# Kernel tuning notes

Hardware: AMD Instinct MI355X
Metric: run time of the kernel (lower is better)

The kernel has to match this reference:

```python
import jax, jax.numpy as jnp
import numpy as np

E = 768
NH_REG = 6   # num_heads - cultural_heads
NH_CUL = 2   # cultural_heads


def _branch(x, wq, bq, wk, bk, wv, bv, wo, bo, cb, nh, mask_add):
    # x: [B,T,E]; weights stored as [in,out]; cb: [1,nh,1,hd]
    B, T, Edim = x.shape
    hd = Edim // nh
    scale = hd ** -0.5
    q = (x @ wq + bq).reshape(B, T, nh, hd).transpose(0, 2, 1, 3)
    k = (x @ wk + bk).reshape(B, T, nh, hd).transpose(0, 2, 1, 3)
    v = (x @ wv + bv).reshape(B, T, nh, hd).transpose(0, 2, 1, 3)
    q = q + cb  # learned cultural bias added to Q
    scores = jnp.einsum('bhtd,bhsd->bhts', q, k) * scale
    scores = scores + mask_add
    w = jax.nn.softmax(scores, axis=-1)  # dropout omitted (eval mode)
    out = jnp.einsum('bhts,bhsd->bhtd', w, v)
    out = out.transpose(0, 2, 1, 3).reshape(B, T, Edim)
    return out @ wo + bo


def setup_inputs() -> dict:
    key = jax.random.key(0)
    ks = jax.random.split(key, 24)
    B, S = 2, 2048
    d = {
        'hidden_states': jax.random.normal(ks[0], (B, S, E), jnp.float32),
        'cultural_mask': jax.random.normal(ks[1], (B, S, S), jnp.float32),
        'attention_mask': jax.random.normal(ks[2], (B, 1, 1, S), jnp.float32),
    }
    s = E ** -0.5
    names = ['rq_w', 'rk_w', 'rv_w', 'ro_w', 'cq_w', 'ck_w', 'cv_w', 'co_w']
    for i, n in enumerate(names):
        d[n] = jax.random.normal(ks[3 + i], (E, E), jnp.float32) * s
    for i, n in enumerate(['rq_b', 'rk_b', 'rv_b', 'ro_b', 'cq_b', 'ck_b', 'cv_b', 'co_b']):
        d[n] = jax.random.normal(ks[11 + i], (E,), jnp.float32) * 0.02
    d['r_cb'] = jnp.zeros((1, NH_REG, 1, E // NH_REG), jnp.float32)
    d['c_cb'] = jnp.zeros((1, NH_CUL, 1, E // NH_CUL), jnp.float32)
    # NOTE: concat of two branches gives 2E features -> out layer maps 2E -> E
    d['out_w'] = jax.random.normal(ks[19], (2 * E, E), jnp.float32) * (2 * E) ** -0.5
    d['out_b'] = jax.random.normal(ks[20], (E,), jnp.float32) * 0.02
    return d


def reference(hidden_states, cultural_mask, attention_mask,
              rq_w, rk_w, rv_w, ro_w, cq_w, ck_w, cv_w, co_w,
              rq_b, rk_b, rv_b, ro_b, cq_b, ck_b, cv_b, co_b,
              r_cb, c_cb, out_w, out_b):
    # regular branch: attention_mask only
    reg = _branch(hidden_states, rq_w, rq_b, rk_w, rk_b, rv_w, rv_b,
                  ro_w, ro_b, r_cb, NH_REG, attention_mask)
    # cultural branch: cultural_mask (broadcast over heads) + attention_mask
    cmask = cultural_mask[:, None, :, :] + attention_mask
    cul = _branch(hidden_states, cq_w, cq_b, ck_w, ck_b, cv_w, cv_b,
                  co_w, co_b, c_cb, NH_CUL, cmask)
    combined = jnp.concatenate([reg, cul], axis=-1)  # [B,T,2E]
    return combined @ out_w + out_b
```

## Files before the change

kernel.cpp:

```cpp
#include <hip/hip_runtime.h>
#include <hip/hip_bf16.h>

using u16 = unsigned short;
using u32 = unsigned int;
typedef short short8 __attribute__((ext_vector_type(8)));
typedef float f32x4 __attribute__((ext_vector_type(4)));

#define B_  2
#define S_  2048
#define E_  768
#define BS_ 4096

#define L2E_ 1.44269504088896f
#define FML2_ 17.3123404906676f

__device__ __forceinline__ u16 f2bf(float f) {
  __hip_bfloat16 h = __float2bfloat16(f);
  return *reinterpret_cast<u16*>(&h);
}

__device__ __forceinline__ u32 pk2(float a, float b) {
  return (u32)f2bf(a) | ((u32)f2bf(b) << 16);
}

__device__ __forceinline__ void gld16(const void* g, void* l) {
  __builtin_amdgcn_global_load_lds(
      (const __attribute__((address_space(1))) u32*)g,
      (__attribute__((address_space(3))) u32*)l, 16, 0, 0);
}


__global__ __launch_bounds__(256) void conv_x_k(const float* __restrict__ x,
                                                u16* __restrict__ xb, int n4) {
  int i = blockIdx.x * 256 + threadIdx.x;
  if (i >= n4) return;
  float4 v = reinterpret_cast<const float4*>(x)[i];
  reinterpret_cast<uint2*>(xb)[i] = make_uint2(pk2(v.x, v.y), pk2(v.z, v.w));
}

__global__ __launch_bounds__(256) void bias_k(
    const float* rqb, const float* rkb, const float* rvb,
    const float* cqb, const float* ckb, const float* cvb,
    const float* rob, const float* cob,
    const float* rcb, const float* ccb,
    float* bqkv, float* bproj) {
  int t = blockIdx.x * 256 + threadIdx.x;
  if (t < 4608) {
    int seg = t / 768, i = t - seg * 768;
    float v = 0.f;
    if      (seg == 0) v = rqb[i] + rcb[i];
    else if (seg == 1) v = rkb[i];
    else if (seg == 2) v = rvb[i];
    else if (seg == 3) v = cqb[i] + ccb[i];
    else if (seg == 4) v = ckb[i];
    else               v = cvb[i];
    bqkv[t] = v;
  } else {
    int u = t - 4608;
    if (u < 1536) bproj[u] = (u < 768) ? rob[u] : cob[u - 768];
  }
}

struct TP {
  const float* src[9];
  u16* dst[9];
  int rows[9];
};

__global__ __launch_bounds__(256) void transpose_k(TP p) {
  int mi = blockIdx.z;
  int rows = p.rows[mi];
  int r0 = blockIdx.y * 32;
  if (r0 >= rows) return;
  int c0 = blockIdx.x * 32;
  const float* src = p.src[mi];
  u16* dst = p.dst[mi];
  __shared__ float t[32][33];
  int tx = threadIdx.x & 31, ty = threadIdx.x >> 5;
#pragma unroll
  for (int d = 0; d < 4; ++d) {
    int r = ty + d * 8;
    t[r][tx] = src[(size_t)(r0 + r) * 768 + c0 + tx];
  }
  __syncthreads();
#pragma unroll
  for (int d = 0; d < 4; ++d) {
    int c = ty + d * 8;
    dst[(size_t)(c0 + c) * rows + r0 + tx] = f2bf(t[tx][c]);
  }
}


template<int MODE>
__global__ __launch_bounds__(256) void gemm_t_k(
    const u16* __restrict__ A, int lda,
    const u16* __restrict__ BT, int ldb,
    const float* __restrict__ bias, int K,
    const u16* __restrict__ A2, int msplit, int bofs,
    void* __restrict__ Cout, int ldc,
    u16* __restrict__ Qr, u16* __restrict__ Kr, u16* __restrict__ Vtr,
    u16* __restrict__ Qc, u16* __restrict__ Kc, u16* __restrict__ Vtc) {
  __shared__ u16 lA[128 * 32];
  __shared__ u16 lB[128 * 32];
  const int tid = threadIdx.x, w = tid >> 6, lane = tid & 63;
  const int quad = lane >> 4, l15 = lane & 15;
  const int m0 = blockIdx.y * 128, n0 = blockIdx.x * 128;
  if (msplit && m0 >= msplit) { A = A2 - (size_t)msplit * lda; BT += bofs; }

  const f32x4 z4 = {0.f, 0.f, 0.f, 0.f};
  f32x4 acc[4][4];
#pragma unroll
  for (int i = 0; i < 4; ++i)
#pragma unroll
    for (int j = 0; j < 4; ++j) acc[i][j] = z4;

  const int sr = w * 32 + (lane >> 2);
  const int scp = lane & 3;

  for (int kt = 0; kt < K; kt += 32) {
    int r1 = sr, r2 = sr + 16;
    int c1 = (scp - (r1 >> 2)) & 3;
    int c2 = (scp - (r2 >> 2)) & 3;
    gld16(A + (size_t)(m0 + r1) * lda + kt + c1 * 8, &lA[r1 * 32 + scp * 8]);
    gld16(A + (size_t)(m0 + r2) * lda + kt + c2 * 8, &lA[r2 * 32 + scp * 8]);
    gld16(BT + (size_t)(n0 + r1) * ldb + kt + c1 * 8, &lB[r1 * 32 + scp * 8]);
    gld16(BT + (size_t)(n0 + r2) * ldb + kt + c2 * 8, &lB[r2 * 32 + scp * 8]);
    __syncthreads();
    short8 af[4], bg[4];
#pragma unroll
    for (int i = 0; i < 4; ++i) {
      int r = (w >> 1) * 64 + i * 16 + l15;
      af[i] = *reinterpret_cast<const short8*>(&lA[r * 32 + ((quad + (r >> 2)) & 3) * 8]);
    }
#pragma unroll
    for (int j = 0; j < 4; ++j) {
      int r = (w & 1) * 64 + j * 16 + l15;
      bg[j] = *reinterpret_cast<const short8*>(&lB[r * 32 + ((quad + (r >> 2)) & 3) * 8]);
    }
#pragma unroll
    for (int i = 0; i < 4; ++i)
#pragma unroll
      for (int j = 0; j < 4; ++j)
        acc[i][j] = __builtin_amdgcn_mfma_f32_16x16x32_bf16(af[i], bg[j], acc[i][j], 0, 0, 0);
    __syncthreads();
  }

  const int seg = (MODE == 2) ? (m0 / 768) : 0;
#pragma unroll
  for (int i = 0; i < 4; ++i) {
    int f = m0 + (w >> 1) * 64 + i * 16 + quad * 4;
    float4 b4 = *reinterpret_cast<const float4*>(bias + f);
#pragma unroll
    for (int j = 0; j < 4; ++j) {
      int t = n0 + (w & 1) * 64 + j * 16 + l15;
      float v0 = acc[i][j][0] + b4.x;
      float v1 = acc[i][j][1] + b4.y;
      float v2 = acc[i][j][2] + b4.z;
      float v3 = acc[i][j][3] + b4.w;
      if (MODE == 0) {
        *reinterpret_cast<uint2*>((u16*)Cout + (size_t)t * ldc + f) =
            make_uint2(pk2(v0, v1), pk2(v2, v3));
      } else if (MODE == 1) {
        *reinterpret_cast<float4*>((float*)Cout + (size_t)t * ldc + f) =
            make_float4(v0, v1, v2, v3);
      } else {
        int b = t >> 11, s = t & 2047;
        int fs = f - seg * 768;
        if (seg == 0) {
          int h = fs >> 7, d = fs & 127;
          *reinterpret_cast<uint2*>(Qr + ((size_t)(b * 6 + h) * 2048 + s) * 128 + d) =
              make_uint2(pk2(v0, v1), pk2(v2, v3));
        } else if (seg == 1) {
          int h = fs >> 7, d = fs & 127;
          *reinterpret_cast<uint2*>(Kr + ((size_t)(b * 6 + h) * 2048 + s) * 128 + d) =
              make_uint2(pk2(v0, v1), pk2(v2, v3));
        } else if (seg == 2) {
          int h = fs >> 7, d = fs & 127;
          u16* vp = Vtr + ((size_t)(b * 6 + h) * 128 + d) * 2048 + s;
          vp[0] = f2bf(v0); vp[2048] = f2bf(v1); vp[4096] = f2bf(v2); vp[6144] = f2bf(v3);
        } else if (seg == 3) {
          int h = fs / 384, d = fs - h * 384;
          *reinterpret_cast<uint2*>(Qc + ((size_t)(b * 2 + h) * 2048 + s) * 384 + d) =
              make_uint2(pk2(v0, v1), pk2(v2, v3));
        } else if (seg == 4) {
          int h = fs / 384, d = fs - h * 384;
          *reinterpret_cast<uint2*>(Kc + ((size_t)(b * 2 + h) * 2048 + s) * 384 + d) =
              make_uint2(pk2(v0, v1), pk2(v2, v3));
        } else {
          int h = fs / 384, d = fs - h * 384;
          u16* vp = Vtc + ((size_t)(b * 2 + h) * 384 + d) * 2048 + s;
          vp[0] = f2bf(v0); vp[2048] = f2bf(v1); vp[4096] = f2bf(v2); vp[6144] = f2bf(v3);
        }
      }
    }
  }
}

__global__ __launch_bounds__(256) void attn_freg_k(
    const u16* __restrict__ Qr, const u16* __restrict__ Kr,
    const u16* __restrict__ Vtr, const float* __restrict__ am,
    u16* __restrict__ AO, float scl) {
  __shared__ u16 lQ[64 * 128];
  __shared__ u16 lK[128 * 32];
  __shared__ u16 lV[128 * 32];
  __shared__ u16 lP[64 * 128];
  __shared__ float lL[2][64];

  const int tid = threadIdx.x, w = tid >> 6, lane = tid & 63;
  const int quad = lane >> 4, l15 = lane & 15;
  const int L = blockIdx.x;
  const int gg = (L & 7) * 48 + (L >> 3);
  const int bh = gg >> 5;
  const int q0 = (gg & 31) * 64;
  const int b = bh / 6, h = bh - b * 6;

  const u16* Qb = Qr + ((size_t)bh * S_ + q0) * 128;
  const u16* Kb0 = Kr + (size_t)bh * S_ * 128;
  const u16* Vb0 = Vtr + (size_t)bh * 128 * S_;
  const float* amb = am + b * S_;

#pragma unroll
  for (int it = 0; it < 4; ++it) {
    int idx = it * 256 + tid;
    int row = idx >> 4, gs = idx & 15;
    gld16(Qb + (size_t)row * 128 + (size_t)(gs ^ (row & 15)) * 8, &lQ[idx * 8]);
  }

  const f32x4 z4 = {0.f, 0.f, 0.f, 0.f};
  f32x4 accO[4][2];
#pragma unroll
  for (int i = 0; i < 4; ++i)
#pragma unroll
    for (int j = 0; j < 2; ++j) accO[i][j] = z4;
  float lsum[2] = {0.f, 0.f};

  const int sr = w * 32 + (lane >> 2);
  const int scp = lane & 3;
  const int r1 = sr, r2 = sr + 16;
  const int c1 = (scp - (r1 >> 2)) & 3;
  const int c2 = (scp - (r2 >> 2)) & 3;
  const int khalf = w >> 1, qhalf = w & 1;

  for (int t = 0; t < 16; ++t) {
    const u16* Kb = Kb0 + (size_t)(t * 128) * 128;
    f32x4 accS[4][2];
#pragma unroll
    for (int i = 0; i < 4; ++i)
#pragma unroll
      for (int j = 0; j < 2; ++j) accS[i][j] = z4;

#pragma unroll
    for (int c = 0; c < 4; ++c) {
      gld16(Kb + (size_t)r1 * 128 + c * 32 + c1 * 8, &lK[r1 * 32 + scp * 8]);
      gld16(Kb + (size_t)r2 * 128 + c * 32 + c2 * 8, &lK[r2 * 32 + scp * 8]);
      __syncthreads();
      short8 af[4], bg[2];
#pragma unroll
      for (int i = 0; i < 4; ++i) {
        int r = khalf * 64 + i * 16 + l15;
        af[i] = *reinterpret_cast<const short8*>(&lK[r * 32 + ((quad + (r >> 2)) & 3) * 8]);
      }
#pragma unroll
      for (int j = 0; j < 2; ++j) {
        int q = qhalf * 32 + j * 16 + l15;
        int s = (4 * c + quad) ^ (q & 15);
        bg[j] = *reinterpret_cast<const short8*>(&lQ[q * 128 + s * 8]);
      }
#pragma unroll
      for (int i = 0; i < 4; ++i)
#pragma unroll
        for (int j = 0; j < 2; ++j)
          accS[i][j] = __builtin_amdgcn_mfma_f32_16x16x32_bf16(af[i], bg[j], accS[i][j], 0, 0, 0);
      __syncthreads();
    }

#pragma unroll
    for (int i = 0; i < 4; ++i) {
      int kb = khalf * 64 + i * 16 + quad * 4;
      float4 a4 = *reinterpret_cast<const float4*>(amb + t * 128 + kb);
      float p0c = fmaf(a4.x, L2E_, -FML2_);
      float p1c = fmaf(a4.y, L2E_, -FML2_);
      float p2c = fmaf(a4.z, L2E_, -FML2_);
      float p3c = fmaf(a4.w, L2E_, -FML2_);
      int sg = (kb >> 3) ^ 0;
      int so = kb & 7;
#pragma unroll
      for (int j = 0; j < 2; ++j) {
        int q = qhalf * 32 + j * 16 + l15;
        float p0 = exp2f(fmaf(accS[i][j][0], scl, p0c));
        float p1 = exp2f(fmaf(accS[i][j][1], scl, p1c));
        float p2 = exp2f(fmaf(accS[i][j][2], scl, p2c));
        float p3 = exp2f(fmaf(accS[i][j][3], scl, p3c));
        lsum[j] += (p0 + p1) + (p2 + p3);
        int s = ((kb >> 3) ^ (q & 15));
        *reinterpret_cast<uint2*>(&lP[q * 128 + s * 8 + so]) =
            make_uint2(pk2(p0, p1), pk2(p2, p3));
      }
      (void)sg;
    }
    __syncthreads();

    const u16* Vb = Vb0 + t * 128;
#pragma unroll
    for (int c = 0; c < 4; ++c) {
      gld16(Vb + (size_t)r1 * S_ + c * 32 + c1 * 8, &lV[r1 * 32 + scp * 8]);
      gld16(Vb + (size_t)r2 * S_ + c * 32 + c2 * 8, &lV[r2 * 32 + scp * 8]);
      __syncthreads();
      short8 af[4], bg[2];
#pragma unroll
      for (int i = 0; i < 4; ++i) {
        int r = khalf * 64 + i * 16 + l15;
        af[i] = *reinterpret_cast<const short8*>(&lV[r * 32 + ((quad + (r >> 2)) & 3) * 8]);
      }
#pragma unroll
      for (int j = 0; j < 2; ++j) {
        int q = qhalf * 32 + j * 16 + l15;
        int s = (4 * c + quad) ^ (q & 15);
        bg[j] = *reinterpret_cast<const short8*>(&lP[q * 128 + s * 8]);
      }
#pragma unroll
      for (int i = 0; i < 4; ++i)
#pragma unroll
        for (int j = 0; j < 2; ++j)
          accO[i][j] = __builtin_amdgcn_mfma_f32_16x16x32_bf16(af[i], bg[j], accO[i][j], 0, 0, 0);
      __syncthreads();
    }
  }

#pragma unroll
  for (int j = 0; j < 2; ++j) {
    float s = lsum[j];
    s += __shfl_xor(s, 16);
    s += __shfl_xor(s, 32);
    if (lane < 16) lL[khalf][qhalf * 32 + j * 16 + lane] = s;
  }
  __syncthreads();

  float invl[2];
#pragma unroll
  for (int j = 0; j < 2; ++j) {
    int q = qhalf * 32 + j * 16 + l15;
    invl[j] = 1.f / (lL[0][q] + lL[1][q]);
  }
#pragma unroll
  for (int i = 0; i < 4; ++i) {
    int d = khalf * 64 + i * 16 + quad * 4;
#pragma unroll
    for (int j = 0; j < 2; ++j) {
      int tok = q0 + qhalf * 32 + j * 16 + l15;
      float v0 = accO[i][j][0] * invl[j];
      float v1 = accO[i][j][1] * invl[j];
      float v2 = accO[i][j][2] * invl[j];
      float v3 = accO[i][j][3] * invl[j];
      *reinterpret_cast<uint2*>(AO + ((size_t)(b * S_ + tok)) * 1536 + h * 128 + d) =
          make_uint2(pk2(v0, v1), pk2(v2, v3));
    }
  }
}

__global__ __launch_bounds__(256) void attn_g1_k(
    const u16* __restrict__ Qr, const u16* __restrict__ Kr,
    const u16* __restrict__ Qc, const u16* __restrict__ Kc,
    u16* __restrict__ Pr, u16* __restrict__ Pc, float* __restrict__ Lp,
    const float* __restrict__ am, const float* __restrict__ cmask,
    float sReg, float sCul, int zoff) {
  __shared__ u16 lA[128 * 32];
  __shared__ u16 lB[128 * 32];
  const int tid = threadIdx.x, w = tid >> 6, lane = tid & 63;
  const int quad = lane >> 4, l15 = lane & 15;
  const int m0 = blockIdx.y * 128, n0 = blockIdx.x * 128;
  const int gz = zoff + blockIdx.z;
  const u16 *A, *BT;
  u16* P;
  const float* cm = nullptr;
  float scl;
  int K, b;
  if (gz < 12) {
    A = Kr + (size_t)gz * S_ * 128;
    BT = Qr + (size_t)gz * S_ * 128;
    K = 128;
    P = Pr + (size_t)blockIdx.z * (size_t)S_ * S_;
    scl = sReg;
    b = gz / 6;
  } else {
    int hc = gz - 12;
    A = Kc + (size_t)hc * S_ * 384;
    BT = Qc + (size_t)hc * S_ * 384;
    K = 384;
    P = Pc + (size_t)hc * (size_t)S_ * S_;
    b = hc >> 1;
    cm = cmask + (size_t)b * S_ * S_;
    scl = sCul;
  }

  const f32x4 z4 = {0.f, 0.f, 0.f, 0.f};
  f32x4 acc[4][4];
#pragma unroll
  for (int i = 0; i < 4; ++i)
#pragma unroll
    for (int j = 0; j < 4; ++j) acc[i][j] = z4;

  const int sr = w * 32 + (lane >> 2);
  const int scp = lane & 3;

  for (int kt = 0; kt < K; kt += 32) {
    int r1 = sr, r2 = sr + 16;
    int c1 = (scp - (r1 >> 2)) & 3;
    int c2 = (scp - (r2 >> 2)) & 3;
    gld16(A + (size_t)(m0 + r1) * K + kt + c1 * 8, &lA[r1 * 32 + scp * 8]);
    gld16(A + (size_t)(m0 + r2) * K + kt + c2 * 8, &lA[r2 * 32 + scp * 8]);
    gld16(BT + (size_t)(n0 + r1) * K + kt + c1 * 8, &lB[r1 * 32 + scp * 8]);
    gld16(BT + (size_t)(n0 + r2) * K + kt + c2 * 8, &lB[r2 * 32 + scp * 8]);
    __syncthreads();
    short8 af[4], bg[4];
#pragma unroll
    for (int i = 0; i < 4; ++i) {
      int r = (w >> 1) * 64 + i * 16 + l15;
      af[i] = *reinterpret_cast<const short8*>(&lA[r * 32 + ((quad + (r >> 2)) & 3) * 8]);
    }
#pragma unroll
    for (int j = 0; j < 4; ++j) {
      int r = (w & 1) * 64 + j * 16 + l15;
      bg[j] = *reinterpret_cast<const short8*>(&lB[r * 32 + ((quad + (r >> 2)) & 3) * 8]);
    }
#pragma unroll
    for (int i = 0; i < 4; ++i)
#pragma unroll
      for (int j = 0; j < 4; ++j)
        acc[i][j] = __builtin_amdgcn_mfma_f32_16x16x32_bf16(af[i], bg[j], acc[i][j], 0, 0, 0);
    __syncthreads();
  }

  const float* amb = am + b * S_;
  float lsum[4] = {0.f, 0.f, 0.f, 0.f};
#pragma unroll
  for (int i = 0; i < 4; ++i) {
    int kb = m0 + (w >> 1) * 64 + i * 16 + quad * 4;
    float4 a4 = *reinterpret_cast<const float4*>(amb + kb);
    float pre0 = fmaf(a4.x, L2E_, -FML2_);
    float pre1 = fmaf(a4.y, L2E_, -FML2_);
    float pre2 = fmaf(a4.z, L2E_, -FML2_);
    float pre3 = fmaf(a4.w, L2E_, -FML2_);
#pragma unroll
    for (int j = 0; j < 4; ++j) {
      int q = n0 + (w & 1) * 64 + j * 16 + l15;
      float c0 = pre0, c1 = pre1, c2 = pre2, c3 = pre3;
      if (cm) {
        float4 cmv = *reinterpret_cast<const float4*>(cm + (size_t)q * S_ + kb);
        c0 = fmaf(cmv.x, L2E_, c0);
        c1 = fmaf(cmv.y, L2E_, c1);
        c2 = fmaf(cmv.z, L2E_, c2);
        c3 = fmaf(cmv.w, L2E_, c3);
      }
      float p0 = exp2f(fmaf(acc[i][j][0], scl, c0));
      float p1 = exp2f(fmaf(acc[i][j][1], scl, c1));
      float p2 = exp2f(fmaf(acc[i][j][2], scl, c2));
      float p3 = exp2f(fmaf(acc[i][j][3], scl, c3));
      lsum[j] += (p0 + p1) + (p2 + p3);
      *reinterpret_cast<uint2*>(P + (size_t)q * S_ + kb) =
          make_uint2(pk2(p0, p1), pk2(p2, p3));
    }
  }
#pragma unroll
  for (int j = 0; j < 4; ++j) {
    float s = lsum[j];
    s += __shfl_xor(s, 16);
    s += __shfl_xor(s, 32);
    if (lane < 16)
      Lp[(size_t)gz * (32 * S_) + ((size_t)((m0 >> 7) * 2 + (w >> 1))) * S_ +
         n0 + (w & 1) * 64 + j * 16 + lane] = s;
  }
}

__global__ __launch_bounds__(256) void attn_g2_k(
    const u16* __restrict__ Pr, const u16* __restrict__ Pc,
    const u16* __restrict__ Vtr, const u16* __restrict__ Vtc,
    const float* __restrict__ Lp, u16* __restrict__ AO, int zoff) {
  const int gz = zoff + blockIdx.z;
  const int m0 = blockIdx.y * 128, n0 = blockIdx.x * 128;
  const u16 *A, *BT;
  int b, colbase;
  if (gz < 12) {
    if (blockIdx.y) return;
    A = Vtr + (size_t)gz * 128 * S_;
    BT = Pr + (size_t)blockIdx.z * (size_t)S_ * S_;
    b = gz / 6;
    colbase = (gz % 6) * 128;
  } else {
    int hc = gz - 12;
    A = Vtc + (size_t)hc * 384 * S_;
    BT = Pc + (size_t)hc * (size_t)S_ * S_;
    b = hc >> 1;
    colbase = 768 + (hc & 1) * 384;
  }
  __shared__ u16 lA[128 * 32];
  __shared__ u16 lB[128 * 32];
  __shared__ float lL[128];
  const int tid = threadIdx.x, w = tid >> 6, lane = tid & 63;
  const int quad = lane >> 4, l15 = lane & 15;

  if (tid < 128) {
    const float* lp = Lp + (size_t)gz * (32 * S_) + (n0 + tid);
    float s = 0.f;
#pragma unroll
    for (int g = 0; g < 32; ++g) s += lp[(size_t)g * S_];
    lL[tid] = 1.f / s;
  }

  const f32x4 z4 = {0.f, 0.f, 0.f, 0.f};
  f32x4 acc[4][4];
#pragma unroll
  for (int i = 0; i < 4; ++i)
#pragma unroll
    for (int j = 0; j < 4; ++j) acc[i][j] = z4;

  const int sr = w * 32 + (lane >> 2);
  const int scp = lane & 3;

  for (int kt = 0; kt < S_; kt += 32) {
    int r1 = sr, r2 = sr + 16;
    int c1 = (scp - (r1 >> 2)) & 3;
    int c2 = (scp - (r2 >> 2)) & 3;
    gld16(A + (size_t)(m0 + r1) * S_ + kt + c1 * 8, &lA[r1 * 32 + scp * 8]);
    gld16(A + (size_t)(m0 + r2) * S_ + kt + c2 * 8, &lA[r2 * 32 + scp * 8]);
    gld16(BT + (size_t)(n0 + r1) * S_ + kt + c1 * 8, &lB[r1 * 32 + scp * 8]);
    gld16(BT + (size_t)(n0 + r2) * S_ + kt + c2 * 8, &lB[r2 * 32 + scp * 8]);
    __syncthreads();
    short8 af[4], bg[4];
#pragma unroll
    for (int i = 0; i < 4; ++i) {
      int r = (w >> 1) * 64 + i * 16 + l15;
      af[i] = *reinterpret_cast<const short8*>(&lA[r * 32 + ((quad + (r >> 2)) & 3) * 8]);
    }
#pragma unroll
    for (int j = 0; j < 4; ++j) {
      int r = (w & 1) * 64 + j * 16 + l15;
      bg[j] = *reinterpret_cast<const short8*>(&lB[r * 32 + ((quad + (r >> 2)) & 3) * 8]);
    }
#pragma unroll
    for (int i = 0; i < 4; ++i)
#pragma unroll
      for (int j = 0; j < 4; ++j)
        acc[i][j] = __builtin_amdgcn_mfma_f32_16x16x32_bf16(af[i], bg[j], acc[i][j], 0, 0, 0);
    __syncthreads();
  }

  float invl[4];
#pragma unroll
  for (int j = 0; j < 4; ++j) invl[j] = lL[(w & 1) * 64 + j * 16 + l15];
#pragma unroll
  for (int i = 0; i < 4; ++i) {
    int feat = colbase + m0 + (w >> 1) * 64 + i * 16 + quad * 4;
#pragma unroll
    for (int j = 0; j < 4; ++j) {
      int q = n0 + (w & 1) * 64 + j * 16 + l15;
      float v0 = acc[i][j][0] * invl[j];
      float v1 = acc[i][j][1] * invl[j];
      float v2 = acc[i][j][2] * invl[j];
      float v3 = acc[i][j][3] * invl[j];
      *reinterpret_cast<uint2*>(AO + ((size_t)(b * S_ + q)) * 1536 + feat) =
          make_uint2(pk2(v0, v1), pk2(v2, v3));
    }
  }
}


extern "C" void kernel_launch(void* const* d_in, const int* in_sizes, int n_in,
                              void* d_out, int out_size, void* d_ws, size_t ws_size,
                              hipStream_t stream) {
  const float* x     = (const float*)d_in[0];
  const float* cmask = (const float*)d_in[1];
  const float* amask = (const float*)d_in[2];
  const float* W[8]  = { (const float*)d_in[3], (const float*)d_in[4], (const float*)d_in[5],
                         (const float*)d_in[6], (const float*)d_in[7], (const float*)d_in[8],
                         (const float*)d_in[9], (const float*)d_in[10] };
  const float* rq_b = (const float*)d_in[11];
  const float* rk_b = (const float*)d_in[12];
  const float* rv_b = (const float*)d_in[13];
  const float* ro_b = (const float*)d_in[14];
  const float* cq_b = (const float*)d_in[15];
  const float* ck_b = (const float*)d_in[16];
  const float* cv_b = (const float*)d_in[17];
  const float* co_b = (const float*)d_in[18];
  const float* r_cb = (const float*)d_in[19];
  const float* c_cb = (const float*)d_in[20];
  const float* out_w = (const float*)d_in[21];
  const float* out_b = (const float*)d_in[22];

  char* p = (char*)d_ws;
  auto carve = [&](size_t bytes) -> void* {
    void* r = (void*)p;
    p += (bytes + 255) & ~(size_t)255;
    return r;
  };
  u16* Xb    = (u16*)carve((size_t)BS_ * E_ * 2);
  u16* WqkvT = (u16*)carve((size_t)4608 * 768 * 2);
  u16* roT   = (u16*)carve((size_t)768 * 768 * 2);
  u16* coT   = (u16*)carve((size_t)768 * 768 * 2);
  u16* outwT = (u16*)carve((size_t)768 * 1536 * 2);
  float* bqkv  = (float*)carve(4608 * 4);
  float* bproj = (float*)carve(1536 * 4);
  u16* Qr  = (u16*)carve((size_t)B_ * 6 * S_ * 128 * 2);
  u16* Kr  = (u16*)carve((size_t)B_ * 6 * S_ * 128 * 2);
  u16* Vtr = (u16*)carve((size_t)B_ * 6 * S_ * 128 * 2);
  u16* Qc  = (u16*)carve((size_t)B_ * 2 * S_ * 384 * 2);
  u16* Kc  = (u16*)carve((size_t)B_ * 2 * S_ * 384 * 2);
  u16* Vtc = (u16*)carve((size_t)B_ * 2 * S_ * 384 * 2);
  u16* AO  = (u16*)carve((size_t)BS_ * 1536 * 2);

  float* Lp = (float*)Xb;
  u16* Pcul = (u16*)carve((size_t)4 * S_ * S_ * 2);
  u16* PR = Pcul;

  const float sReg = 0.08838834764831845f * L2E_;
  const float sCul = 0.05103103630798288f * L2E_;

  conv_x_k<<<dim3(BS_ * E_ / 4 / 256), 256, 0, stream>>>(x, Xb, BS_ * E_ / 4);
  bias_k<<<dim3(24), 256, 0, stream>>>(rq_b, rk_b, rv_b, cq_b, ck_b, cv_b,
                                       ro_b, co_b, r_cb, c_cb, bqkv, bproj);

  TP tp;
  const int wsel[6] = {0, 1, 2, 4, 5, 6};
  for (int i = 0; i < 6; ++i) {
    tp.src[i] = W[wsel[i]];
    tp.dst[i] = WqkvT + (size_t)i * 768 * 768;
    tp.rows[i] = 768;
  }
  tp.src[6] = W[3]; tp.dst[6] = roT;   tp.rows[6] = 768;
  tp.src[7] = W[7]; tp.dst[7] = coT;   tp.rows[7] = 768;
  tp.src[8] = out_w; tp.dst[8] = outwT; tp.rows[8] = 1536;
  transpose_k<<<dim3(24, 48, 9), 256, 0, stream>>>(tp);

  gemm_t_k<2><<<dim3(32, 36), 256, 0, stream>>>(
      WqkvT, 768, Xb, 768, bqkv, 768,
      (const u16*)nullptr, 0, 0, (void*)nullptr, 0,
      Qr, Kr, Vtr, Qc, Kc, Vtc);

  attn_freg_k<<<dim3(384), 256, 0, stream>>>(Qr, Kr, Vtr, amask, AO, sReg);

  attn_g1_k<<<dim3(16, 16, 4), 256, 0, stream>>>(
      Qr, Kr, Qc, Kc, (u16*)nullptr, Pcul, Lp, amask, cmask, sReg, sCul, 12);
  attn_g2_k<<<dim3(16, 3, 4), 256, 0, stream>>>(
      (const u16*)nullptr, Pcul, Vtr, Vtc, Lp, AO, 12);

  gemm_t_k<0><<<dim3(32, 12), 256, 0, stream>>>(
      roT, 768, AO, 1536, bproj, 768,
      coT, 768, 768, (void*)PR, 1536,
      nullptr, nullptr, nullptr, nullptr, nullptr, nullptr);

  gemm_t_k<1><<<dim3(32, 6), 256, 0, stream>>>(
      outwT, 1536, PR, 1536, out_b, 1536,
      (const u16*)nullptr, 0, 0, d_out, 768,
      nullptr, nullptr, nullptr, nullptr, nullptr, nullptr);
}
```

Before: 426.7 us.

## Fold output projections into final weight and load regular-attention fragments from global

```diff
diff --git a/kernel.cpp b/kernel.cpp
--- a/kernel.cpp
+++ b/kernel.cpp
@@ -17,6 +17,11 @@
 __device__ __forceinline__ u16 f2bf(float f) {
   __hip_bfloat16 h = __float2bfloat16(f);
   return *reinterpret_cast<u16*>(&h);
+}
+
+__device__ __forceinline__ float bf2f(u16 b) {
+  u32 bits = (u32)b << 16;
+  return *reinterpret_cast<float*>(&bits);
 }
 
 __device__ __forceinline__ u32 pk2(float a, float b) {
@@ -38,12 +43,26 @@
   reinterpret_cast<uint2*>(xb)[i] = make_uint2(pk2(v.x, v.y), pk2(v.z, v.w));
 }
 
+__global__ __launch_bounds__(256) void conv_w_k(const float* __restrict__ ro,
+                                                const float* __restrict__ co,
+                                                u16* __restrict__ roB,
+                                                u16* __restrict__ coB) {
+  const int n4 = 768 * 768 / 4;
+  int i = blockIdx.x * 256 + threadIdx.x;
+  const float* src = (i < n4) ? ro : co;
+  u16* dst = (i < n4) ? roB : coB;
+  int k = (i < n4) ? i : i - n4;
+  if (k >= n4) return;
+  float4 v = reinterpret_cast<const float4*>(src)[k];
+  reinterpret_cast<uint2*>(dst)[k] = make_uint2(pk2(v.x, v.y), pk2(v.z, v.w));
+}
+
 __global__ __launch_bounds__(256) void bias_k(
     const float* rqb, const float* rkb, const float* rvb,
     const float* cqb, const float* ckb, const float* cvb,
     const float* rob, const float* cob,
     const float* rcb, const float* ccb,
-    float* bqkv, float* bproj) {
+    float* bqkv, float* bproj, float* zb) {
   int t = blockIdx.x * 256 + threadIdx.x;
   if (t < 4608) {
     int seg = t / 768, i = t - seg * 768;
@@ -55,10 +74,29 @@
     else if (seg == 4) v = ckb[i];
     else               v = cvb[i];
     bqkv[t] = v;
-  } else {
+  } else if (t < 6144) {
     int u = t - 4608;
-    if (u < 1536) bproj[u] = (u < 768) ? rob[u] : cob[u - 768];
-  }
+    bproj[u] = (u < 768) ? rob[u] : cob[u - 768];
+  } else if (t < 6912) {
+    zb[t - 6144] = 0.f;
+  }
+}
+
+__global__ __launch_bounds__(64) void bfin_k(
+    const float* __restrict__ bproj, const u16* __restrict__ outwT,
+    const float* __restrict__ outb, float* __restrict__ bfin) {
+  int o = blockIdx.x;
+  int lane = threadIdx.x;
+  const u16* row = outwT + (size_t)o * 1536;
+  float s = 0.f;
+  for (int i = lane; i < 1536; i += 64) s += bproj[i] * bf2f(row[i]);
+  s += __shfl_xor(s, 1);
+  s += __shfl_xor(s, 2);
+  s += __shfl_xor(s, 4);
+  s += __shfl_xor(s, 8);
+  s += __shfl_xor(s, 16);
+  s += __shfl_xor(s, 32);
+  if (lane == 0) bfin[o] = s + outb[o];
 }
 
 struct TP {
@@ -200,9 +238,6 @@
     const u16* __restrict__ Qr, const u16* __restrict__ Kr,
     const u16* __restrict__ Vtr, const float* __restrict__ am,
     u16* __restrict__ AO, float scl) {
-  __shared__ u16 lQ[64 * 128];
-  __shared__ u16 lK[128 * 32];
-  __shared__ u16 lV[128 * 32];
   __shared__ u16 lP[64 * 128];
   __shared__ float lL[2][64];
 
@@ -213,18 +248,20 @@
   const int bh = gg >> 5;
   const int q0 = (gg & 31) * 64;
   const int b = bh / 6, h = bh - b * 6;
+  const int khalf = w >> 1, qhalf = w & 1;
 
   const u16* Qb = Qr + ((size_t)bh * S_ + q0) * 128;
   const u16* Kb0 = Kr + (size_t)bh * S_ * 128;
   const u16* Vb0 = Vtr + (size_t)bh * 128 * S_;
   const float* amb = am + b * S_;
 
-#pragma unroll
-  for (int it = 0; it < 4; ++it) {
-    int idx = it * 256 + tid;
-    int row = idx >> 4, gs = idx & 15;
-    gld16(Qb + (size_t)row * 128 + (size_t)(gs ^ (row & 15)) * 8, &lQ[idx * 8]);
-  }
+  short8 qf[2][4];
+#pragma unroll
+  for (int j = 0; j < 2; ++j)
+#pragma unroll
+    for (int c = 0; c < 4; ++c)
+      qf[j][c] = *reinterpret_cast<const short8*>(
+          Qb + (size_t)(qhalf * 32 + j * 16 + l15) * 128 + c * 32 + quad * 8);
 
   const f32x4 z4 = {0.f, 0.f, 0.f, 0.f};
   f32x4 accO[4][2];
@@ -234,45 +271,28 @@
     for (int j = 0; j < 2; ++j) accO[i][j] = z4;
   float lsum[2] = {0.f, 0.f};
 
-  const int sr = w * 32 + (lane >> 2);
-  const int scp = lane & 3;
-  const int r1 = sr, r2 = sr + 16;
-  const int c1 = (scp - (r1 >> 2)) & 3;
-  const int c2 = (scp - (r2 >> 2)) & 3;
-  const int khalf = w >> 1, qhalf = w & 1;
-
   for (int t = 0; t < 16; ++t) {
-    const u16* Kb = Kb0 + (size_t)(t * 128) * 128;
     f32x4 accS[4][2];
 #pragma unroll
     for (int i = 0; i < 4; ++i)
 #pragma unroll
       for (int j = 0; j < 2; ++j) accS[i][j] = z4;
-
+    const u16* Kt = Kb0 + (size_t)t * 128 * 128;
 #pragma unroll
     for (int c = 0; c < 4; ++c) {
-      gld16(Kb + (size_t)r1 * 128 + c * 32 + c1 * 8, &lK[r1 * 32 + scp * 8]);
-      gld16(Kb + (size_t)r2 * 128 + c * 32 + c2 * 8, &lK[r2 * 32 + scp * 8]);
-      __syncthreads();
-      short8 af[4], bg[2];
-#pragma unroll
-      for (int i = 0; i < 4; ++i) {
-        int r = khalf * 64 + i * 16 + l15;
-        af[i] = *reinterpret_cast<const short8*>(&lK[r * 32 + ((quad + (r >> 2)) & 3) * 8]);
-      }
-#pragma unroll
-      for (int j = 0; j < 2; ++j) {
-        int q = qhalf * 32 + j * 16 + l15;
-        int s = (4 * c + quad) ^ (q & 15);
-        bg[j] = *reinterpret_cast<const short8*>(&lQ[q * 128 + s * 8]);
-      }
+      short8 kf[4];
 #pragma unroll
       for (int i = 0; i < 4; ++i)
+        kf[i] = *reinterpret_cast<const short8*>(
+            Kt + (size_t)(khalf * 64 + i * 16 + l15) * 128 + c * 32 + quad * 8);
+#pragma unroll
+      for (int i = 0; i < 4; ++i)
 #pragma unroll
         for (int j = 0; j < 2; ++j)
-          accS[i][j] = __builtin_amdgcn_mfma_f32_16x16x32_bf16(af[i], bg[j], accS[i][j], 0, 0, 0);
-      __syncthreads();
-    }
+          accS[i][j] = __builtin_amdgcn_mfma_f32_16x16x32_bf16(kf[i], qf[j][c], accS[i][j], 0, 0, 0);
+    }
+
+    __syncthreads();
 
 #pragma unroll
     for (int i = 0; i < 4; ++i) {
@@ -282,8 +302,6 @@
       float p1c = fmaf(a4.y, L2E_, -FML2_);
       float p2c = fmaf(a4.z, L2E_, -FML2_);
       float p3c = fmaf(a4.w, L2E_, -FML2_);
-      int sg = (kb >> 3) ^ 0;
-      int so = kb & 7;
 #pragma unroll
       for (int j = 0; j < 2; ++j) {
         int q = qhalf * 32 + j * 16 + l15;
@@ -293,25 +311,20 @@
         float p3 = exp2f(fmaf(accS[i][j][3], scl, p3c));
         lsum[j] += (p0 + p1) + (p2 + p3);
         int s = ((kb >> 3) ^ (q & 15));
-        *reinterpret_cast<uint2*>(&lP[q * 128 + s * 8 + so]) =
+        *reinterpret_cast<uint2*>(&lP[q * 128 + s * 8 + (kb & 7)]) =
             make_uint2(pk2(p0, p1), pk2(p2, p3));
       }
-      (void)sg;
-    }
-    __syncthreads();
-
-    const u16* Vb = Vb0 + t * 128;
+    }
+    __syncthreads();
+
 #pragma unroll
     for (int c = 0; c < 4; ++c) {
-      gld16(Vb + (size_t)r1 * S_ + c * 32 + c1 * 8, &lV[r1 * 32 + scp * 8]);
-      gld16(Vb + (size_t)r2 * S_ + c * 32 + c2 * 8, &lV[r2 * 32 + scp * 8]);
-      __syncthreads();
-      short8 af[4], bg[2];
-#pragma unroll
-      for (int i = 0; i < 4; ++i) {
-        int r = khalf * 64 + i * 16 + l15;
-        af[i] = *reinterpret_cast<const short8*>(&lV[r * 32 + ((quad + (r >> 2)) & 3) * 8]);
-      }
+      short8 vf[4];
+#pragma unroll
+      for (int i = 0; i < 4; ++i)
+        vf[i] = *reinterpret_cast<const short8*>(
+            Vb0 + (size_t)(khalf * 64 + i * 16 + l15) * S_ + t * 128 + c * 32 + quad * 8);
+      short8 bg[2];
 #pragma unroll
       for (int j = 0; j < 2; ++j) {
         int q = qhalf * 32 + j * 16 + l15;
@@ -322,8 +335,7 @@
       for (int i = 0; i < 4; ++i)
 #pragma unroll
         for (int j = 0; j < 2; ++j)
-          accO[i][j] = __builtin_amdgcn_mfma_f32_16x16x32_bf16(af[i], bg[j], accO[i][j], 0, 0, 0);
-      __syncthreads();
+          accO[i][j] = __builtin_amdgcn_mfma_f32_16x16x32_bf16(vf[i], bg[j], accO[i][j], 0, 0, 0);
     }
   }
 
@@ -359,39 +371,23 @@
 }
 
 __global__ __launch_bounds__(256) void attn_g1_k(
-    const u16* __restrict__ Qr, const u16* __restrict__ Kr,
     const u16* __restrict__ Qc, const u16* __restrict__ Kc,
-    u16* __restrict__ Pr, u16* __restrict__ Pc, float* __restrict__ Lp,
+    u16* __restrict__ Pc, float* __restrict__ Lp,
     const float* __restrict__ am, const float* __restrict__ cmask,
-    float sReg, float sCul, int zoff) {
+    float sCul) {
   __shared__ u16 lA[128 * 32];
   __shared__ u16 lB[128 * 32];
   const int tid = threadIdx.x, w = tid >> 6, lane = tid & 63;
   const int quad = lane >> 4, l15 = lane & 15;
   const int m0 = blockIdx.y * 128, n0 = blockIdx.x * 128;
-  const int gz = zoff + blockIdx.z;
-  const u16 *A, *BT;
-  u16* P;
-  const float* cm = nullptr;
-  float scl;
-  int K, b;
-  if (gz < 12) {
-    A = Kr + (size_t)gz * S_ * 128;
-    BT = Qr + (size_t)gz * S_ * 128;
-    K = 128;
-    P = Pr + (size_t)blockIdx.z * (size_t)S_ * S_;
-    scl = sReg;
-    b = gz / 6;
-  } else {
-    int hc = gz - 12;
-    A = Kc + (size_t)hc * S_ * 384;
-    BT = Qc + (size_t)hc * S_ * 384;
-    K = 384;
-    P = Pc + (size_t)hc * (size_t)S_ * S_;
-    b = hc >> 1;
-    cm = cmask + (size_t)b * S_ * S_;
-    scl = sCul;
-  }
+  const int hc = blockIdx.z;
+  const int K = 384;
+  const u16* A = Kc + (size_t)hc * S_ * 384;
+  const u16* BT = Qc + (size_t)hc * S_ * 384;
+  u16* P = Pc + (size_t)hc * (size_t)S_ * S_;
+  const int b = hc >> 1;
+  const float* cm = cmask + (size_t)b * S_ * S_;
+  const float scl = sCul;
 
   const f32x4 z4 = {0.f, 0.f, 0.f, 0.f};
   f32x4 acc[4][4];
@@ -444,14 +440,11 @@
 #pragma unroll
     for (int j = 0; j < 4; ++j) {
       int q = n0 + (w & 1) * 64 + j * 16 + l15;
-      float c0 = pre0, c1 = pre1, c2 = pre2, c3 = pre3;
-      if (cm) {
-        float4 cmv = *reinterpret_cast<const float4*>(cm + (size_t)q * S_ + kb);
-        c0 = fmaf(cmv.x, L2E_, c0);
-        c1 = fmaf(cmv.y, L2E_, c1);
-        c2 = fmaf(cmv.z, L2E_, c2);
-        c3 = fmaf(cmv.w, L2E_, c3);
-      }
+      float4 cmv = *reinterpret_cast<const float4*>(cm + (size_t)q * S_ + kb);
+      float c0 = fmaf(cmv.x, L2E_, pre0);
+      float c1 = fmaf(cmv.y, L2E_, pre1);
+      float c2 = fmaf(cmv.z, L2E_, pre2);
+      float c3 = fmaf(cmv.w, L2E_, pre3);
       float p0 = exp2f(fmaf(acc[i][j][0], scl, c0));
       float p1 = exp2f(fmaf(acc[i][j][1], scl, c1));
       float p2 = exp2f(fmaf(acc[i][j][2], scl, c2));
@@ -467,32 +460,20 @@
     s += __shfl_xor(s, 16);
     s += __shfl_xor(s, 32);
     if (lane < 16)
-      Lp[(size_t)gz * (32 * S_) + ((size_t)((m0 >> 7) * 2 + (w >> 1))) * S_ +
+      Lp[(size_t)hc * (32 * S_) + ((size_t)((m0 >> 7) * 2 + (w >> 1))) * S_ +
          n0 + (w & 1) * 64 + j * 16 + lane] = s;
   }
 }
 
 __global__ __launch_bounds__(256) void attn_g2_k(
-    const u16* __restrict__ Pr, const u16* __restrict__ Pc,
-    const u16* __restrict__ Vtr, const u16* __restrict__ Vtc,
-    const float* __restrict__ Lp, u16* __restrict__ AO, int zoff) {
-  const int gz = zoff + blockIdx.z;
+    const u16* __restrict__ Pc, const u16* __restrict__ Vtc,
+    const float* __restrict__ Lp, u16* __restrict__ AO) {
+  const int hc = blockIdx.z;
   const int m0 = blockIdx.y * 128, n0 = blockIdx.x * 128;
-  const u16 *A, *BT;
-  int b, colbase;
-  if (gz < 12) {
-    if (blockIdx.y) return;
-    A = Vtr + (size_t)gz * 128 * S_;
-    BT = Pr + (size_t)blockIdx.z * (size_t)S_ * S_;
-    b = gz / 6;
-    colbase = (gz % 6) * 128;
-  } else {
-    int hc = gz - 12;
-    A = Vtc + (size_t)hc * 384 * S_;
-    BT = Pc + (size_t)hc * (size_t)S_ * S_;
-    b = hc >> 1;
-    colbase = 768 + (hc & 1) * 384;
-  }
+  const u16* A = Vtc + (size_t)hc * 384 * S_;
+  const u16* BT = Pc + (size_t)hc * (size_t)S_ * S_;
+  const int b = hc >> 1;
+  const int colbase = 768 + (hc & 1) * 384;
   __shared__ u16 lA[128 * 32];
   __shared__ u16 lB[128 * 32];
   __shared__ float lL[128];
@@ -500,7 +481,7 @@
   const int quad = lane >> 4, l15 = lane & 15;
 
   if (tid < 128) {
-    const float* lp = Lp + (size_t)gz * (32 * S_) + (n0 + tid);
+    const float* lp = Lp + (size_t)hc * (32 * S_) + (n0 + tid);
     float s = 0.f;
 #pragma unroll
     for (int g = 0; g < 32; ++g) s += lp[(size_t)g * S_];
@@ -595,11 +576,14 @@
   };
   u16* Xb    = (u16*)carve((size_t)BS_ * E_ * 2);
   u16* WqkvT = (u16*)carve((size_t)4608 * 768 * 2);
-  u16* roT   = (u16*)carve((size_t)768 * 768 * 2);
-  u16* coT   = (u16*)carve((size_t)768 * 768 * 2);
+  u16* roB   = (u16*)carve((size_t)768 * 768 * 2);
+  u16* coB   = (u16*)carve((size_t)768 * 768 * 2);
   u16* outwT = (u16*)carve((size_t)768 * 1536 * 2);
+  u16* WfT   = (u16*)carve((size_t)768 * 1536 * 2);
   float* bqkv  = (float*)carve(4608 * 4);
   float* bproj = (float*)carve(1536 * 4);
+  float* zb    = (float*)carve(768 * 4);
+  float* bfin  = (float*)carve(768 * 4);
   u16* Qr  = (u16*)carve((size_t)B_ * 6 * S_ * 128 * 2);
   u16* Kr  = (u16*)carve((size_t)B_ * 6 * S_ * 128 * 2);
   u16* Vtr = (u16*)carve((size_t)B_ * 6 * S_ * 128 * 2);
@@ -607,17 +591,16 @@
   u16* Kc  = (u16*)carve((size_t)B_ * 2 * S_ * 384 * 2);
   u16* Vtc = (u16*)carve((size_t)B_ * 2 * S_ * 384 * 2);
   u16* AO  = (u16*)carve((size_t)BS_ * 1536 * 2);
-
+  u16* Pcul = (u16*)carve((size_t)4 * S_ * S_ * 2);
   float* Lp = (float*)Xb;
-  u16* Pcul = (u16*)carve((size_t)4 * S_ * S_ * 2);
-  u16* PR = Pcul;
 
   const float sReg = 0.08838834764831845f * L2E_;
   const float sCul = 0.05103103630798288f * L2E_;
 
   conv_x_k<<<dim3(BS_ * E_ / 4 / 256), 256, 0, stream>>>(x, Xb, BS_ * E_ / 4);
-  bias_k<<<dim3(24), 256, 0, stream>>>(rq_b, rk_b, rv_b, cq_b, ck_b, cv_b,
-                                       ro_b, co_b, r_cb, c_cb, bqkv, bproj);
+  conv_w_k<<<dim3(2 * 768 * 768 / 4 / 256), 256, 0, stream>>>(W[3], W[7], roB, coB);
+  bias_k<<<dim3(27), 256, 0, stream>>>(rq_b, rk_b, rv_b, cq_b, ck_b, cv_b,
+                                       ro_b, co_b, r_cb, c_cb, bqkv, bproj, zb);
 
   TP tp;
   const int wsel[6] = {0, 1, 2, 4, 5, 6};
@@ -626,10 +609,10 @@
     tp.dst[i] = WqkvT + (size_t)i * 768 * 768;
     tp.rows[i] = 768;
   }
-  tp.src[6] = W[3]; tp.dst[6] = roT;   tp.rows[6] = 768;
-  tp.src[7] = W[7]; tp.dst[7] = coT;   tp.rows[7] = 768;
+  tp.src[6] = out_w; tp.dst[6] = outwT; tp.rows[6] = 1536;
+  tp.src[7] = out_w; tp.dst[7] = outwT; tp.rows[7] = 1536;
   tp.src[8] = out_w; tp.dst[8] = outwT; tp.rows[8] = 1536;
-  transpose_k<<<dim3(24, 48, 9), 256, 0, stream>>>(tp);
+  transpose_k<<<dim3(24, 48, 7), 256, 0, stream>>>(tp);
 
   gemm_t_k<2><<<dim3(32, 36), 256, 0, stream>>>(
       WqkvT, 768, Xb, 768, bqkv, 768,
@@ -639,17 +622,21 @@
   attn_freg_k<<<dim3(384), 256, 0, stream>>>(Qr, Kr, Vtr, amask, AO, sReg);
 
   attn_g1_k<<<dim3(16, 16, 4), 256, 0, stream>>>(
-      Qr, Kr, Qc, Kc, (u16*)nullptr, Pcul, Lp, amask, cmask, sReg, sCul, 12);
-  attn_g2_k<<<dim3(16, 3, 4), 256, 0, stream>>>(
-      (const u16*)nullptr, Pcul, Vtr, Vtc, Lp, AO, 12);
-
-  gemm_t_k<0><<<dim3(32, 12), 256, 0, stream>>>(
-      roT, 768, AO, 1536, bproj, 768,
-      coT, 768, 768, (void*)PR, 1536,
+      Qc, Kc, Pcul, Lp, amask, cmask, sCul);
+  attn_g2_k<<<dim3(16, 3, 4), 256, 0, stream>>>(Pcul, Vtc, Lp, AO);
+
+  gemm_t_k<0><<<dim3(6, 6), 256, 0, stream>>>(
+      roB, 768, outwT, 1536, zb, 768,
+      (const u16*)nullptr, 0, 0, (void*)WfT, 1536,
       nullptr, nullptr, nullptr, nullptr, nullptr, nullptr);
+  gemm_t_k<0><<<dim3(6, 6), 256, 0, stream>>>(
+      coB, 768, outwT + 768, 1536, zb, 768,
+      (const u16*)nullptr, 0, 0, (void*)(WfT + 768), 1536,
+      nullptr, nullptr, nullptr, nullptr, nullptr, nullptr);
+  bfin_k<<<dim3(768), 64, 0, stream>>>(bproj, outwT, out_b, bfin);
 
   gemm_t_k<1><<<dim3(32, 6), 256, 0, stream>>>(
-      outwT, 1536, PR, 1536, out_b, 1536,
+      WfT, 1536, AO, 1536, bfin, 1536,
       (const u16*)nullptr, 0, 0, d_out, 768,
       nullptr, nullptr, nullptr, nullptr, nullptr, nullptr);
 }
```

Result: slower. 495.6 us (+16.1%).
